# Performance work log

Hardware: AMD Instinct MI355X
Metric: run time of the kernel (lower is better)

Reference implementation:

```python
import jax, jax.numpy as jnp
import numpy as np

EMBED = 1024
HEADS = 16


def setup_inputs() -> dict:
    key = jax.random.key(0)
    ks = jax.random.split(key, 5)
    N, L, E = 4, 4096, EMBED
    s = 0.02  # weight init scale
    return {
        "x": jax.random.normal(ks[0], (N, L, E), dtype=jnp.float32),
        "Wq": jax.random.normal(ks[1], (E, E), dtype=jnp.float32) * s,
        "Wk": jax.random.normal(ks[2], (E, E), dtype=jnp.float32) * s,
        "Wv": jax.random.normal(ks[3], (E, E), dtype=jnp.float32) * s,
        "Wo": jax.random.normal(ks[4], (E, E), dtype=jnp.float32) * s,
        "bo": jnp.zeros((E,), dtype=jnp.float32),
    }


def reference(x, Wq, Wk, Wv, Wo, bo):
    # Faithful translation of the torch module, INCLUDING its permute/einsum quirk:
    # after permute, q/k/v are (N, H, L, D) and einsum 'nqhd,nkhd->nqk' contracts
    # over length (h) and head_dim (d), yielding an (N, H, H) energy tensor.
    N, L, E = x.shape
    H = HEADS
    D = E // H

    def proj(W):
        # torch nn.Linear: y = x @ W.T ; then view + permute(0,2,1,3) -> (N,H,L,D)
        y = jnp.einsum('nle,fe->nlf', x, W)
        return y.reshape(N, L, H, D).transpose(0, 2, 1, 3)

    q = proj(Wq)  # (N, H, L, D)
    k = proj(Wk)
    v = proj(Wv)

    energy = jnp.einsum('nqhd,nkhd->nqk', q, k)  # (N, H, H): contracts L and D
    attention = jax.nn.softmax(energy / jnp.sqrt(jnp.float32(E)), axis=2)
    # 'nqk,nvhd->nqhd': k summed in attention only, v summed in values only
    out = jnp.einsum('nqk,nvhd->nqhd', attention, v)  # (N, H, L, D)
    out = out.reshape(N, L, H * D)  # layout-scrambling reshape, as in torch
    return jnp.einsum('nle,fe->nlf', out, Wo) + bo
```

## Files before the change

kernel.cpp:

```cpp
#include <hip/hip_runtime.h>
#include <hip/hip_bf16.h>


typedef unsigned short u16;
typedef __attribute__((ext_vector_type(8))) short  short8v;
typedef __attribute__((ext_vector_type(4))) float  f32x4;
typedef __attribute__((ext_vector_type(4))) u16    ushort4v;

__device__ __forceinline__ u16 f2bf(float f) {
    unsigned u = __float_as_uint(f);
    u += 0x7fffu + ((u >> 16) & 1u);
    return (u16)(u >> 16);
}
__device__ __forceinline__ float bf2f(u16 h) {
    return __uint_as_float(((unsigned)h) << 16);
}
__device__ __forceinline__ f32x4 mfma16(short8v a, short8v b, f32x4 c) {
    return __builtin_amdgcn_mfma_f32_16x16x32_bf16(a, b, c, 0, 0, 0);
}
__device__ __forceinline__ void split8(f32x4 v0, f32x4 v1, short8v& h8, short8v& l8) {
    float wf[8] = {v0[0],v0[1],v0[2],v0[3],v1[0],v1[1],v1[2],v1[3]};
#pragma unroll
    for (int j = 0; j < 8; ++j) {
        u16 hh = f2bf(wf[j]);
        h8[j] = (short)hh;
        l8[j] = (short)f2bf(wf[j] - bf2f(hh));
    }
}

__global__ __launch_bounds__(256) void k_pack(const float* __restrict__ Wv,
                                              const float* __restrict__ Wo,
                                              u16* __restrict__ Bh, u16* __restrict__ Bl,
                                              u16* __restrict__ Woh, u16* __restrict__ Wol) {
    const int b = blockIdx.x;
    if (b < 512) {
        const int g = b * 256 + threadIdx.x;
        const f32x4* p = (const f32x4*)(Wo + (size_t)g * 8);
        short8v h8, l8; split8(p[0], p[1], h8, l8);
        ((short8v*)Woh)[g] = h8;
        ((short8v*)Wol)[g] = l8;
    } else {
        const int t  = (b - 512) * 256 + threadIdx.x;
        const int c  = t >> 7;
        const int e8 = t & 127;
        f32x4 s0 = {0,0,0,0}, s1 = {0,0,0,0};
#pragma unroll
        for (int h = 0; h < 16; ++h) {
            const f32x4* p = (const f32x4*)&Wv[(size_t)((h << 6) + c) * 1024 + (e8 << 3)];
            s0 += p[0]; s1 += p[1];
        }
        short8v h8, l8; split8(s0, s1, h8, l8);
        ((short8v*)Bh)[e8 * 64 + c] = h8;
        ((short8v*)Bl)[e8 * 64 + c] = l8;
    }
}

__global__ __launch_bounds__(256, 4) void k_vsum(const float* __restrict__ x,
                                                 const u16* __restrict__ Bh,
                                                 const u16* __restrict__ Bl,
                                                 u16* __restrict__ Zh,
                                                 u16* __restrict__ Zl) {
    __shared__ float red[4][64][16];
    const int t = threadIdx.x, lane = t & 63, w = t >> 6;
    const int l15 = lane & 15, lh = lane >> 4;
    const int g = blockIdx.x;
    const int R0 = g << 4;
    const int kbase = w << 8;
    const short8v* bh8 = (const short8v*)Bh;
    const short8v* bl8 = (const short8v*)Bl;

    f32x4 acc[4] = {{0,0,0,0},{0,0,0,0},{0,0,0,0},{0,0,0,0}};

#pragma unroll 2
    for (int kt = 0; kt < 8; ++kt) {
        const int k0 = kbase + (kt << 5);
        const float* ap = &x[(size_t)(R0 + l15) * 1024 + k0 + (lh << 3)];
        f32x4 a0 = __builtin_nontemporal_load((const f32x4*)ap);
        f32x4 a1 = __builtin_nontemporal_load((const f32x4*)(ap + 4));
        short8v ah, al; split8(a0, a1, ah, al);
        const int e8 = (k0 >> 3) + lh;
#pragma unroll
        for (int cg = 0; cg < 4; ++cg) {
            short8v bh = bh8[e8 * 64 + (cg << 4) + l15];
            short8v bl = bl8[e8 * 64 + (cg << 4) + l15];
            acc[cg] = mfma16(ah, bh, acc[cg]);
            acc[cg] = mfma16(ah, bl, acc[cg]);
            acc[cg] = mfma16(al, bh, acc[cg]);
        }
    }

#pragma unroll
    for (int cg = 0; cg < 4; ++cg)
#pragma unroll
        for (int reg = 0; reg < 4; ++reg)
            red[w][lane][(cg << 2) + reg] = acc[cg][reg];
    __syncthreads();

    ushort4v zh, zl;
#pragma unroll
    for (int j = 0; j < 4; ++j) {
        const int e = (t << 2) + j, v15 = e >> 6, c = e & 63;
        const int ln = ((v15 >> 2) << 4) | (c & 15);
        const int slot = ((c >> 4) << 2) | (v15 & 3);
        float s = red[0][ln][slot] + red[1][ln][slot] + red[2][ln][slot] + red[3][ln][slot];
        u16 hh = f2bf(s);
        zh[j] = hh;
        zl[j] = f2bf(s - bf2f(hh));
    }
    *(ushort4v*)&Zh[((size_t)g << 10) + (t << 2)] = zh;
    *(ushort4v*)&Zl[((size_t)g << 10) + (t << 2)] = zl;
}

__global__ __launch_bounds__(512, 2) void k_ugemm(const u16* __restrict__ Zh,
                                                  const u16* __restrict__ Zl,
                                                  const u16* __restrict__ Woh,
                                                  const u16* __restrict__ Wol,
                                                  const float* __restrict__ bo,
                                                  float* __restrict__ out) {
    __shared__ float red[8][64][16];
    const int t = threadIdx.x, lane = t & 63, w = t >> 6;
    const int l15 = lane & 15, lh = lane >> 4;
    const int rg = w & 3, kh = w >> 2;
    const int rt = blockIdx.x & 15, ct = blockIdx.x >> 4;
    const int rbase = (rt << 6) + (rg << 4), fbase = ct << 6;

    f32x4 acc[4] = {{0,0,0,0},{0,0,0,0},{0,0,0,0},{0,0,0,0}};
    const size_t arow = (size_t)(rbase + l15) << 10;

#pragma unroll 2
    for (int kt = 0; kt < 16; ++kt) {
        const int k0 = (kh << 9) + (kt << 5) + (lh << 3);
        short8v ah = *(const short8v*)&Zh[arow + k0];
        short8v al = *(const short8v*)&Zl[arow + k0];
#pragma unroll
        for (int cg = 0; cg < 4; ++cg) {
            const size_t brow = (size_t)(fbase + (cg << 4) + l15) << 10;
            short8v bh = *(const short8v*)&Woh[brow + k0];
            short8v bl = *(const short8v*)&Wol[brow + k0];
            acc[cg] = mfma16(ah, bh, acc[cg]);
            acc[cg] = mfma16(ah, bl, acc[cg]);
            acc[cg] = mfma16(al, bh, acc[cg]);
        }
    }

#pragma unroll
    for (int cg = 0; cg < 4; ++cg)
#pragma unroll
        for (int reg = 0; reg < 4; ++reg)
            red[w][lane][(cg << 2) + reg] = acc[cg][reg];
    __syncthreads();

    const int r = t >> 3, cbase = (t & 7) << 3;
    const int rg2 = r >> 4, lh2 = (r & 15) >> 2, reg2 = r & 3;
    const int ur = (rt << 6) + r;
    const int n = ur >> 8, m = ur & 255;
    float* ob = out + ((size_t)n << 22) + ((size_t)m << 10) + fbase + cbase;
#pragma unroll
    for (int jj = 0; jj < 2; ++jj) {
        f32x4 o;
#pragma unroll
        for (int q = 0; q < 4; ++q) {
            const int c = cbase + (jj << 2) + q;
            const int ln = (lh2 << 4) | (c & 15);
            const int slot = ((c >> 4) << 2) | reg2;
            o[q] = red[rg2][ln][slot] + red[4 + rg2][ln][slot] + bo[fbase + c];
        }
        *(f32x4*)(ob + (jj << 2)) = o;
    }
}

__global__ __launch_bounds__(256) void k_bcast(float* __restrict__ out) {
    const int T = blockIdx.x * 256 + threadIdx.x;
    const int f4 = T & 255, m = (T >> 8) & 255, n = T >> 16;
    float* src = out + ((size_t)n << 22) + ((size_t)m << 10) + (f4 << 2);
    f32x4 v = *(const f32x4*)src;
#pragma unroll
    for (int q = 1; q < 16; ++q)
        __builtin_nontemporal_store(v, (f32x4*)(src + ((size_t)q << 18)));
}

extern "C" void kernel_launch(void* const* d_in, const int* in_sizes, int n_in,
                              void* d_out, int out_size, void* d_ws, size_t ws_size,
                              hipStream_t stream) {
    const float* x  = (const float*)d_in[0];
    const float* Wv = (const float*)d_in[3];
    const float* Wo = (const float*)d_in[4];
    const float* bo = (const float*)d_in[5];
    float* out = (float*)d_out;

    u16* Bh = (u16*)d_ws;
    u16* Bl = Bh + 64 * 1024;

    u16* Woh = (u16*)(out + (size_t)14 * 1024 * 1024);
    u16* Wol = Woh + 1024 * 1024;
    u16* Zh  = Wol + 1024 * 1024;
    u16* Zl  = Zh  + 1024 * 1024;

    k_pack <<<544,  256, 0, stream>>>(Wv, Wo, Bh, Bl, Woh, Wol);
    k_vsum <<<1024, 256, 0, stream>>>(x, Bh, Bl, Zh, Zl);
    k_ugemm<<<256,  512, 0, stream>>>(Zh, Zl, Woh, Wol, bo, out);
    k_bcast<<<1024, 256, 0, stream>>>(out);
}
```

Baseline: 190.5 us.

## Pre-pack Wo into k-major fragment layout and retile ugemm to 16-row blocks

The Wo bf16 hi/lo split is now stored transposed into an e8-major layout, so each lane's B-fragment load in the output GEMM is contiguous across lanes instead of strided by 1 KiB rows. The GEMM kernel is retiled from 512-thread blocks covering 64 rows with two k-halves to 256-thread blocks covering 16 rows, with four waves each taking a quarter of K and reducing through padded shared memory. Grid size grows from 256 to 1024 blocks. The aim is better coalescing and more parallelism, at the cost of re-reading each Wo tile for four times as many row blocks.

```diff
diff --git a/kernel.cpp b/kernel.cpp
--- a/kernel.cpp
+++ b/kernel.cpp
@@ -31,14 +31,16 @@
 __global__ __launch_bounds__(256) void k_pack(const float* __restrict__ Wv,
                                               const float* __restrict__ Wo,
                                               u16* __restrict__ Bh, u16* __restrict__ Bl,
-                                              u16* __restrict__ Woh, u16* __restrict__ Wol) {
+                                              u16* __restrict__ Wph, u16* __restrict__ Wpl) {
     const int b = blockIdx.x;
     if (b < 512) {
-        const int g = b * 256 + threadIdx.x;
-        const f32x4* p = (const f32x4*)(Wo + (size_t)g * 8);
+        const int g  = b * 256 + threadIdx.x;
+        const int f  = g & 1023;
+        const int e8 = g >> 10;
+        const f32x4* p = (const f32x4*)(Wo + (size_t)f * 1024 + (e8 << 3));
         short8v h8, l8; split8(p[0], p[1], h8, l8);
-        ((short8v*)Woh)[g] = h8;
-        ((short8v*)Wol)[g] = l8;
+        ((short8v*)Wph)[e8 * 1024 + f] = h8;
+        ((short8v*)Wpl)[e8 * 1024 + f] = l8;
     } else {
         const int t  = (b - 512) * 256 + threadIdx.x;
         const int c  = t >> 7;
@@ -111,32 +113,35 @@
     *(ushort4v*)&Zl[((size_t)g << 10) + (t << 2)] = zl;
 }
 
-__global__ __launch_bounds__(512, 2) void k_ugemm(const u16* __restrict__ Zh,
+__global__ __launch_bounds__(256, 4) void k_ugemm(const u16* __restrict__ Zh,
                                                   const u16* __restrict__ Zl,
-                                                  const u16* __restrict__ Woh,
-                                                  const u16* __restrict__ Wol,
+                                                  const u16* __restrict__ Wph,
+                                                  const u16* __restrict__ Wpl,
                                                   const float* __restrict__ bo,
                                                   float* __restrict__ out) {
-    __shared__ float red[8][64][16];
+    __shared__ float red[4][64][17];
     const int t = threadIdx.x, lane = t & 63, w = t >> 6;
     const int l15 = lane & 15, lh = lane >> 4;
-    const int rg = w & 3, kh = w >> 2;
-    const int rt = blockIdx.x & 15, ct = blockIdx.x >> 4;
-    const int rbase = (rt << 6) + (rg << 4), fbase = ct << 6;
+    const int rt = blockIdx.x & 63, ct = blockIdx.x >> 6;
+    const int rbase = rt << 4;
+    const int fbase = ct << 6;
+    const int kwave = w << 8;
+    const short8v* bph = (const short8v*)Wph;
+    const short8v* bpl = (const short8v*)Wpl;
 
     f32x4 acc[4] = {{0,0,0,0},{0,0,0,0},{0,0,0,0},{0,0,0,0}};
     const size_t arow = (size_t)(rbase + l15) << 10;
 
 #pragma unroll 2
-    for (int kt = 0; kt < 16; ++kt) {
-        const int k0 = (kh << 9) + (kt << 5) + (lh << 3);
-        short8v ah = *(const short8v*)&Zh[arow + k0];
-        short8v al = *(const short8v*)&Zl[arow + k0];
+    for (int kt = 0; kt < 8; ++kt) {
+        const int k0 = kwave + (kt << 5);
+        short8v ah = *(const short8v*)&Zh[arow + k0 + (lh << 3)];
+        short8v al = *(const short8v*)&Zl[arow + k0 + (lh << 3)];
+        const int e8 = (k0 >> 3) + lh;
 #pragma unroll
         for (int cg = 0; cg < 4; ++cg) {
-            const size_t brow = (size_t)(fbase + (cg << 4) + l15) << 10;
-            short8v bh = *(const short8v*)&Woh[brow + k0];
-            short8v bl = *(const short8v*)&Wol[brow + k0];
+            short8v bh = bph[e8 * 1024 + fbase + (cg << 4) + l15];
+            short8v bl = bpl[e8 * 1024 + fbase + (cg << 4) + l15];
             acc[cg] = mfma16(ah, bh, acc[cg]);
             acc[cg] = mfma16(ah, bl, acc[cg]);
             acc[cg] = mfma16(al, bh, acc[cg]);
@@ -150,23 +155,21 @@
             red[w][lane][(cg << 2) + reg] = acc[cg][reg];
     __syncthreads();
 
-    const int r = t >> 3, cbase = (t & 7) << 3;
-    const int rg2 = r >> 4, lh2 = (r & 15) >> 2, reg2 = r & 3;
-    const int ur = (rt << 6) + r;
+    const int i0 = t << 2;
+    const int r  = i0 >> 6;
+    const int cb = i0 & 63;
+    f32x4 o;
+#pragma unroll
+    for (int j = 0; j < 4; ++j) {
+        const int c = cb + j;
+        const int ln = ((r >> 2) << 4) | (c & 15);
+        const int slot = ((c >> 4) << 2) | (r & 3);
+        o[j] = red[0][ln][slot] + red[1][ln][slot] + red[2][ln][slot] + red[3][ln][slot]
+             + bo[fbase + c];
+    }
+    const int ur = rbase + r;
     const int n = ur >> 8, m = ur & 255;
-    float* ob = out + ((size_t)n << 22) + ((size_t)m << 10) + fbase + cbase;
-#pragma unroll
-    for (int jj = 0; jj < 2; ++jj) {
-        f32x4 o;
-#pragma unroll
-        for (int q = 0; q < 4; ++q) {
-            const int c = cbase + (jj << 2) + q;
-            const int ln = (lh2 << 4) | (c & 15);
-            const int slot = ((c >> 4) << 2) | reg2;
-            o[q] = red[rg2][ln][slot] + red[4 + rg2][ln][slot] + bo[fbase + c];
-        }
-        *(f32x4*)(ob + (jj << 2)) = o;
-    }
+    *(f32x4*)&out[((size_t)n << 22) + ((size_t)m << 10) + fbase + cb] = o;
 }
 
 __global__ __launch_bounds__(256) void k_bcast(float* __restrict__ out) {
@@ -191,13 +194,13 @@
     u16* Bh = (u16*)d_ws;
     u16* Bl = Bh + 64 * 1024;
 
-    u16* Woh = (u16*)(out + (size_t)14 * 1024 * 1024);
-    u16* Wol = Woh + 1024 * 1024;
-    u16* Zh  = Wol + 1024 * 1024;
+    u16* Wph = (u16*)(out + (size_t)14 * 1024 * 1024);
+    u16* Wpl = Wph + 1024 * 1024;
+    u16* Zh  = Wpl + 1024 * 1024;
     u16* Zl  = Zh  + 1024 * 1024;
 
-    k_pack <<<544,  256, 0, stream>>>(Wv, Wo, Bh, Bl, Woh, Wol);
+    k_pack <<<544,  256, 0, stream>>>(Wv, Wo, Bh, Bl, Wph, Wpl);
     k_vsum <<<1024, 256, 0, stream>>>(x, Bh, Bl, Zh, Zl);
-    k_ugemm<<<256,  512, 0, stream>>>(Zh, Zl, Woh, Wol, bo, out);
+    k_ugemm<<<1024, 256, 0, stream>>>(Zh, Zl, Wph, Wpl, bo, out);
     k_bcast<<<1024, 256, 0, stream>>>(out);
 }
```

Measured after the change: 171.3 us. -10.1%, faster.
